# Kernel optimization log

Measured on AMD Instinct MI355X. Metric: run time of the kernel, lower is better.

The kernel has to match this reference:

```python
import jax, jax.numpy as jnp
import numpy as np

D_MODEL = 1024
D_STATE = 16
D_CONV = 4
BATCH = 2
SEQ = 2048


def setup_inputs() -> dict:
    key = jax.random.key(0)
    ks = jax.random.split(key, 10)
    s = lambda fan_in: 1.0 / np.sqrt(fan_in)
    x = jax.random.normal(ks[0], (BATCH, SEQ, D_MODEL), dtype=jnp.float32)
    W_in = jax.random.normal(ks[1], (D_MODEL, 2 * D_MODEL), dtype=jnp.float32) * s(D_MODEL)
    conv_w = jax.random.normal(ks[2], (D_MODEL, D_CONV), dtype=jnp.float32) * s(D_CONV)
    conv_b = jax.random.normal(ks[3], (D_MODEL,), dtype=jnp.float32) * 0.01
    W_x = jax.random.normal(ks[4], (D_MODEL, 2 * D_STATE), dtype=jnp.float32) * s(D_MODEL)
    W_dt = jax.random.normal(ks[5], (D_MODEL, D_MODEL), dtype=jnp.float32) * s(D_MODEL)
    b_dt = jax.random.normal(ks[6], (D_MODEL,), dtype=jnp.float32) * 0.01
    A_log = jax.random.normal(ks[7], (D_MODEL,), dtype=jnp.float32) * 0.1
    D_param = jnp.ones((D_MODEL,), dtype=jnp.float32)
    W_out = jax.random.normal(ks[8], (D_MODEL, D_MODEL), dtype=jnp.float32) * s(D_MODEL)
    return {"x": x, "W_in": W_in, "conv_w": conv_w, "conv_b": conv_b,
            "W_x": W_x, "W_dt": W_dt, "b_dt": b_dt, "A_log": A_log,
            "D_param": D_param, "W_out": W_out}


def _selective_scan(x, A, dt, B, C):
    # x, dt: [b, l, d]; A: [d]; B, C: [b, l, n]
    b, l, d = x.shape
    n = B.shape[-1]
    h0 = jnp.zeros((b, d, n), dtype=x.dtype)

    def step(h, inp):
        x_t, dt_t, B_t, C_t = inp  # [b,d], [b,d], [b,n], [b,n]
        dA = jnp.exp(dt_t * A)[..., None]            # [b, d, 1]
        h = h * dA + x_t[..., None] * B_t[:, None, :]  # [b, d, n]
        y_t = jnp.einsum('bdn,bn->bd', h, C_t)
        return h, y_t

    xs = (jnp.swapaxes(x, 0, 1), jnp.swapaxes(dt, 0, 1),
          jnp.swapaxes(B, 0, 1), jnp.swapaxes(C, 0, 1))
    _, ys = jax.lax.scan(step, h0, xs)               # ys: [l, b, d]
    return jnp.swapaxes(ys, 0, 1)


def _forward(x, W_in, conv_w, conv_b, W_x, W_dt, b_dt, A_log, D_param, W_out):
    seq_len = x.shape[1]
    xz = x @ W_in                                     # [b, l, 2d]
    x_ssm, z = jnp.split(xz, 2, axis=-1)
    # causal depthwise conv (torch pads both sides then slices -> left pad only)
    xc = jnp.swapaxes(x_ssm, 1, 2)                    # [b, d, l]
    kernel = conv_w[:, None, :]                       # [d, 1, k]
    xc = jax.lax.conv_general_dilated(
        xc, kernel, window_strides=(1,), padding=[(D_CONV - 1, 0)],
        dimension_numbers=('NCH', 'OIH', 'NCH'), feature_group_count=D_MODEL)
    xc = xc + conv_b[None, :, None]
    x_ssm = jnp.swapaxes(xc, 1, 2)[:, :seq_len]       # [b, l, d]
    x_ssm = jax.nn.silu(x_ssm)
    A = -jnp.exp(A_log)
    dt = jax.nn.softplus(x_ssm @ W_dt + b_dt)
    BC = x_ssm @ W_x
    B, C = jnp.split(BC, 2, axis=-1)
    y = _selective_scan(x_ssm, A, dt, B, C)
    y = y + x_ssm * D_param
    y = y * jax.nn.silu(z)
    return y @ W_out


def reference(x, W_in, conv_w, conv_b, W_x, W_dt, b_dt, A_log, D_param, W_out):
    return _forward(x, W_in, conv_w, conv_b, W_x, W_dt, b_dt, A_log, D_param, W_out)
```

## Files before the change

### kernel.cpp

```cpp
#include <hip/hip_runtime.h>
#include <hip/hip_bf16.h>
#include <math.h>

#define D_MODEL 1024
#define D_STATE 16
#define D_CONV  4
#define BATCH   2
#define SEQ     2048
#define MROWS   (BATCH * SEQ)
#define CHUNK   32
#define NCHUNK  (SEQ / CHUNK)

typedef __attribute__((ext_vector_type(8))) short bf16x8;
typedef __attribute__((ext_vector_type(4))) float f32x4;

__device__ __forceinline__ unsigned short f2bf(float f) {
    unsigned int u = __builtin_bit_cast(unsigned int, f);
    u = (u + 0x7fffu + ((u >> 16) & 1u)) >> 16;
    return (unsigned short)u;
}
__device__ __forceinline__ float bf2f(unsigned short u) {
    return __builtin_bit_cast(float, (unsigned int)u << 16);
}
__device__ __forceinline__ float softplus_f(float v) {
    return (v > 20.f) ? v : log1pf(expf(v));
}

__device__ __forceinline__ void gl2lds16(const unsigned short* g, unsigned short* l) {
    __builtin_amdgcn_global_load_lds(
        (__attribute__((address_space(1))) void*)(void*)g,
        (__attribute__((address_space(3))) void*)(void*)l, 16, 0, 0);
}

__global__ __launch_bounds__(256) void cvt_bf16(const float* __restrict__ src,
                                                unsigned short* __restrict__ dst) {
    const size_t i = ((size_t)blockIdx.x * 256 + threadIdx.x) * 8;
    const float4 v0 = *(const float4*)(src + i);
    const float4 v1 = *(const float4*)(src + i + 4);
    bf16x8 o;
    o[0] = (short)f2bf(v0.x); o[1] = (short)f2bf(v0.y);
    o[2] = (short)f2bf(v0.z); o[3] = (short)f2bf(v0.w);
    o[4] = (short)f2bf(v1.x); o[5] = (short)f2bf(v1.y);
    o[6] = (short)f2bf(v1.z); o[7] = (short)f2bf(v1.w);
    *(bf16x8*)(dst + i) = o;
}

__global__ __launch_bounds__(256) void wtrans(const float* __restrict__ W,
                                              unsigned short* __restrict__ Wt,
                                              int K, int N) {
    __shared__ float tile[32][33];
    const int n0 = blockIdx.x * 32, k0 = blockIdx.y * 32;
    const int tx = threadIdx.x & 31, ty = threadIdx.x >> 5;
#pragma unroll
    for (int r = 0; r < 4; ++r)
        tile[ty + r * 8][tx] = W[(size_t)(k0 + ty + r * 8) * N + n0 + tx];
    __syncthreads();
#pragma unroll
    for (int r = 0; r < 4; ++r)
        Wt[(size_t)(n0 + ty + r * 8) * K + k0 + tx] = f2bf(tile[tx][ty + r * 8]);
}

__global__ __launch_bounds__(256) void wx_stage(const float* __restrict__ Wx,
                                                unsigned short* __restrict__ Wt_cat) {
    const int idx = blockIdx.x * 256 + threadIdx.x;
    const int k = idx & 1023;
    const int n = idx >> 10;
    unsigned short v = 0;
    if (n < 32) v = f2bf(Wx[(size_t)k * 32 + n]);
    Wt_cat[(size_t)(1024 + n) * 1024 + k] = v;
}

template <int EPI>
__global__ __launch_bounds__(256) void gemm64(
        const unsigned short* __restrict__ A, const unsigned short* __restrict__ Bt,
        void* __restrict__ Cout, int N, int K,
        const float* __restrict__ bias, const float* __restrict__ alog,
        float* __restrict__ bc) {
    __shared__ unsigned short As[2][64 * 32];
    __shared__ unsigned short Bs[2][128 * 32];

    const int tid  = threadIdx.x;
    const int wave = tid >> 6, lane = tid & 63;
    const int q = lane >> 4, mr = lane & 15;
    const int m0 = blockIdx.y * 64, n0 = blockIdx.x * 128;

    f32x4 acc[4][2];
#pragma unroll
    for (int mi = 0; mi < 4; ++mi)
#pragma unroll
        for (int ni = 0; ni < 2; ++ni) acc[mi][ni] = {0.f, 0.f, 0.f, 0.f};

    const int kb = (tid & 3) * 8;
    const unsigned short* Ag  = A + (size_t)(m0 + (tid >> 2)) * K + kb;
    const unsigned short* Bg0 = Bt + (size_t)(n0 + (tid >> 2)) * K + kb;
    const unsigned short* Bg1 = Bt + (size_t)(n0 + ((tid + 256) >> 2)) * K + kb;
    const int sA = tid * 8, sB0 = tid * 8, sB1 = (tid + 256) * 8;

    const int NK = K >> 5;
    gl2lds16(Ag, As[0] + sA);
    gl2lds16(Bg0, Bs[0] + sB0);
    gl2lds16(Bg1, Bs[0] + sB1);

    for (int i = 0; i < NK; ++i) {
        __syncthreads();
        const int cur = i & 1, nxt = cur ^ 1;
        if (i + 1 < NK) {
            const int ko = (i + 1) * 32;
            gl2lds16(Ag + ko, As[nxt] + sA);
            gl2lds16(Bg0 + ko, Bs[nxt] + sB0);
            gl2lds16(Bg1 + ko, Bs[nxt] + sB1);
        }
        bf16x8 af[4], bfr[2];
#pragma unroll
        for (int mi = 0; mi < 4; ++mi)
            af[mi] = *(const bf16x8*)(As[cur] + (mi * 16 + mr) * 32 + q * 8);
#pragma unroll
        for (int ni = 0; ni < 2; ++ni)
            bfr[ni] = *(const bf16x8*)(Bs[cur] + (wave * 32 + ni * 16 + mr) * 32 + q * 8);
#pragma unroll
        for (int mi = 0; mi < 4; ++mi)
#pragma unroll
            for (int ni = 0; ni < 2; ++ni)
                acc[mi][ni] = __builtin_amdgcn_mfma_f32_16x16x32_bf16(
                    af[mi], bfr[ni], acc[mi][ni], 0, 0, 0);
    }

#pragma unroll
    for (int ni = 0; ni < 2; ++ni) {
        const int col = n0 + wave * 32 + ni * 16 + mr;
        float be = 0.f, al = 0.f;
        if (EPI == 3 && col < 1024) { be = bias[col]; al = alog[col]; }
#pragma unroll
        for (int mi = 0; mi < 4; ++mi) {
            const int row0 = m0 + mi * 16 + q * 4;
#pragma unroll
            for (int r = 0; r < 4; ++r) {
                float v = acc[mi][ni][r];
                const int row = row0 + r;
                if (EPI == 0) {
                    ((float*)Cout)[(size_t)row * N + col] = v;
                } else if (EPI == 2) {
                    ((unsigned short*)Cout)[(size_t)row * N + col] = f2bf(v);
                } else {
                    if (col < 1024) {
                        float dt = softplus_f(v + be);
                        ((float*)Cout)[(size_t)row * 1024 + col] = expf(dt * (-expf(al)));
                    } else if (col < 1056) {
                        bc[(size_t)row * 32 + (col - 1024)] = v;
                    }
                }
            }
        }
    }
}

__global__ __launch_bounds__(256) void conv_silu_kernel(
        const unsigned short* __restrict__ xz, const float* __restrict__ conv_w,
        const float* __restrict__ conv_b, unsigned short* __restrict__ xssm) {
    int idx = blockIdx.x * 256 + threadIdx.x;
    int d4 = idx & 255;
    int bt = idx >> 8;
    int t  = bt & (SEQ - 1);
    int d  = d4 * 4;

    float acc[4];
#pragma unroll
    for (int i = 0; i < 4; ++i) acc[i] = conv_b[d + i];

#pragma unroll
    for (int j = 0; j < D_CONV; ++j) {
        int tt = t - (D_CONV - 1) + j;
        if (tt < 0) continue;
        const ushort4 xv = *(const ushort4*)(&xz[((size_t)(bt - t + tt)) * 2048 + d]);
        acc[0] += bf2f(xv.x) * conv_w[(d + 0) * 4 + j];
        acc[1] += bf2f(xv.y) * conv_w[(d + 1) * 4 + j];
        acc[2] += bf2f(xv.z) * conv_w[(d + 2) * 4 + j];
        acc[3] += bf2f(xv.w) * conv_w[(d + 3) * 4 + j];
    }
    ushort4 o;
    o.x = f2bf(acc[0] / (1.f + expf(-acc[0])));
    o.y = f2bf(acc[1] / (1.f + expf(-acc[1])));
    o.z = f2bf(acc[2] / (1.f + expf(-acc[2])));
    o.w = f2bf(acc[3] / (1.f + expf(-acc[3])));
    *(ushort4*)(&xssm[(size_t)bt * D_MODEL + d]) = o;
}

__global__ __launch_bounds__(256) void scan_pass1(
        const unsigned short* __restrict__ xssm, const float* __restrict__ dAb,
        const float* __restrict__ BCb,
        float* __restrict__ Sbuf, float* __restrict__ Pbuf) {
    const int ch = blockIdx.x, dg = blockIdx.y, b = blockIdx.z;
    const int tid = threadIdx.x;
    const int dd  = dg * 256 + tid;
    const int t0  = ch * CHUNK;

    __shared__ float Bs[CHUNK][16];
    if (tid < CHUNK * 4) {
        const int t = tid >> 2, j = (tid & 3) * 4;
        *(float4*)&Bs[t][j] = *(const float4*)&BCb[((size_t)b * SEQ + t0 + t) * 32 + j];
    }
    __syncthreads();

    const size_t base = ((size_t)b * SEQ + t0) * D_MODEL + dd;
    float h[16];
#pragma unroll
    for (int n = 0; n < 16; ++n) h[n] = 0.f;
    float P = 1.f;

#pragma unroll 2
    for (int t = 0; t < CHUNK; ++t) {
        const float dA = dAb[base + (size_t)t * D_MODEL];
        const float x  = bf2f(xssm[base + (size_t)t * D_MODEL]);
        P *= dA;
        const float4 B0 = *(const float4*)&Bs[t][0];
        const float4 B1 = *(const float4*)&Bs[t][4];
        const float4 B2 = *(const float4*)&Bs[t][8];
        const float4 B3 = *(const float4*)&Bs[t][12];
        h[0]  = h[0]  * dA + x * B0.x;  h[1]  = h[1]  * dA + x * B0.y;
        h[2]  = h[2]  * dA + x * B0.z;  h[3]  = h[3]  * dA + x * B0.w;
        h[4]  = h[4]  * dA + x * B1.x;  h[5]  = h[5]  * dA + x * B1.y;
        h[6]  = h[6]  * dA + x * B1.z;  h[7]  = h[7]  * dA + x * B1.w;
        h[8]  = h[8]  * dA + x * B2.x;  h[9]  = h[9]  * dA + x * B2.y;
        h[10] = h[10] * dA + x * B2.z;  h[11] = h[11] * dA + x * B2.w;
        h[12] = h[12] * dA + x * B3.x;  h[13] = h[13] * dA + x * B3.y;
        h[14] = h[14] * dA + x * B3.z;  h[15] = h[15] * dA + x * B3.w;
    }

    const size_t so = ((size_t)(b * D_MODEL + dd) * NCHUNK + ch) * 16;
#pragma unroll
    for (int n = 0; n < 16; n += 4)
        *(float4*)&Sbuf[so + n] = make_float4(h[n], h[n + 1], h[n + 2], h[n + 3]);
    Pbuf[(size_t)(b * D_MODEL + dd) * NCHUNK + ch] = P;
}

__global__ __launch_bounds__(128) void scan_mid(
        const float* __restrict__ Sbuf, const float* __restrict__ Pbuf,
        float* __restrict__ Hin) {
    const int idx = blockIdx.x * 128 + threadIdx.x;
    const int n   = idx & 15;
    const int dn  = idx >> 4;

    float h = 0.f;
    for (int ch = 0; ch < NCHUNK; ++ch) {
        const size_t s = ((size_t)dn * NCHUNK + ch) * 16 + n;
        Hin[s] = h;
        h = Pbuf[(size_t)dn * NCHUNK + ch] * h + Sbuf[s];
    }
}

__global__ __launch_bounds__(256) void scan_pass2(
        const unsigned short* __restrict__ xssm, const float* __restrict__ dAb,
        const float* __restrict__ BCb, const unsigned short* __restrict__ xz,
        const float* __restrict__ Dp, const float* __restrict__ Hin,
        unsigned short* __restrict__ ybuf) {
    const int ch = blockIdx.x, dg = blockIdx.y, b = blockIdx.z;
    const int tid = threadIdx.x;
    const int dd  = dg * 256 + tid;
    const int t0  = ch * CHUNK;

    __shared__ float BCs[CHUNK][32];
    {
        const int t = tid >> 3, j = (tid & 7) * 4;
        *(float4*)&BCs[t][j] = *(const float4*)&BCb[((size_t)b * SEQ + t0 + t) * 32 + j];
    }
    __syncthreads();

    const float Dpv = Dp[dd];
    const size_t base  = ((size_t)b * SEQ + t0) * D_MODEL + dd;
    const size_t baseZ = ((size_t)b * SEQ + t0) * 2048 + D_MODEL + dd;

    float h[16];
    const size_t ho = ((size_t)(b * D_MODEL + dd) * NCHUNK + ch) * 16;
#pragma unroll
    for (int n = 0; n < 16; n += 4) {
        const float4 hv = *(const float4*)&Hin[ho + n];
        h[n] = hv.x; h[n + 1] = hv.y; h[n + 2] = hv.z; h[n + 3] = hv.w;
    }

#pragma unroll 2
    for (int t = 0; t < CHUNK; ++t) {
        const float dA = dAb[base + (size_t)t * D_MODEL];
        const float x  = bf2f(xssm[base + (size_t)t * D_MODEL]);
        const float4 B0 = *(const float4*)&BCs[t][0];
        const float4 B1 = *(const float4*)&BCs[t][4];
        const float4 B2 = *(const float4*)&BCs[t][8];
        const float4 B3 = *(const float4*)&BCs[t][12];
        const float4 C0 = *(const float4*)&BCs[t][16];
        const float4 C1 = *(const float4*)&BCs[t][20];
        const float4 C2 = *(const float4*)&BCs[t][24];
        const float4 C3 = *(const float4*)&BCs[t][28];
        float y = 0.f;
        h[0]  = h[0]  * dA + x * B0.x;  y += h[0]  * C0.x;
        h[1]  = h[1]  * dA + x * B0.y;  y += h[1]  * C0.y;
        h[2]  = h[2]  * dA + x * B0.z;  y += h[2]  * C0.z;
        h[3]  = h[3]  * dA + x * B0.w;  y += h[3]  * C0.w;
        h[4]  = h[4]  * dA + x * B1.x;  y += h[4]  * C1.x;
        h[5]  = h[5]  * dA + x * B1.y;  y += h[5]  * C1.y;
        h[6]  = h[6]  * dA + x * B1.z;  y += h[6]  * C1.z;
        h[7]  = h[7]  * dA + x * B1.w;  y += h[7]  * C1.w;
        h[8]  = h[8]  * dA + x * B2.x;  y += h[8]  * C2.x;
        h[9]  = h[9]  * dA + x * B2.y;  y += h[9]  * C2.y;
        h[10] = h[10] * dA + x * B2.z;  y += h[10] * C2.z;
        h[11] = h[11] * dA + x * B2.w;  y += h[11] * C2.w;
        h[12] = h[12] * dA + x * B3.x;  y += h[12] * C3.x;
        h[13] = h[13] * dA + x * B3.y;  y += h[13] * C3.y;
        h[14] = h[14] * dA + x * B3.z;  y += h[14] * C3.z;
        h[15] = h[15] * dA + x * B3.w;  y += h[15] * C3.w;

        const float zv = bf2f(xz[baseZ + (size_t)t * 2048]);
        const float sz = zv / (1.f + expf(-zv));
        ybuf[base + (size_t)t * D_MODEL] = f2bf((y + x * Dpv) * sz);
    }
}

extern "C" void kernel_launch(void* const* d_in, const int* in_sizes, int n_in,
                              void* d_out, int out_size, void* d_ws, size_t ws_size,
                              hipStream_t stream) {
    const float* x       = (const float*)d_in[0];
    const float* W_in    = (const float*)d_in[1];
    const float* conv_w  = (const float*)d_in[2];
    const float* conv_b  = (const float*)d_in[3];
    const float* W_x     = (const float*)d_in[4];
    const float* W_dt    = (const float*)d_in[5];
    const float* b_dt    = (const float*)d_in[6];
    const float* A_log   = (const float*)d_in[7];
    const float* D_param = (const float*)d_in[8];
    const float* W_out   = (const float*)d_in[9];
    float* out = (float*)d_out;
    char* ws   = (char*)d_ws;

    unsigned short* xz_bf   = (unsigned short*)(ws + 0);
    unsigned short* xssm_bf = (unsigned short*)(ws + 16777216);
    float*          dAb     = (float*)(ws + 25165824);
    float*          BCb     = (float*)(ws + 41943040);
    unsigned short* ybuf_bf = (unsigned short*)(ws + 42467328);
    unsigned short* xb      = (unsigned short*)(ws + 50855936);
    unsigned short* Wt_in   = (unsigned short*)(ws + 59244544);
    unsigned short* Wt_cat  = (unsigned short*)(ws + 63438848);
    unsigned short* Wt_out  = (unsigned short*)(ws + 65798144);
    float*          Sbuf    = (float*)(ws + 67895296);
    float*          Pbuf    = (float*)(ws + 76283904);
    float*          Hin     = (float*)(ws + 76808192);

    cvt_bf16<<<MROWS * D_MODEL / (256 * 8), 256, 0, stream>>>(x, xb);
    wtrans<<<dim3(2048 / 32, 1024 / 32), 256, 0, stream>>>(W_in, Wt_in, 1024, 2048);
    wtrans<<<dim3(1024 / 32, 1024 / 32), 256, 0, stream>>>(W_dt, Wt_cat, 1024, 1024);
    wx_stage<<<(128 * 1024) / 256, 256, 0, stream>>>(W_x, Wt_cat);
    wtrans<<<dim3(1024 / 32, 1024 / 32), 256, 0, stream>>>(W_out, Wt_out, 1024, 1024);

    gemm64<2><<<dim3(2048 / 128, MROWS / 64), 256, 0, stream>>>(
        xb, Wt_in, xz_bf, 2048, D_MODEL, nullptr, nullptr, nullptr);
    conv_silu_kernel<<<(MROWS * 256) / 256, 256, 0, stream>>>(xz_bf, conv_w, conv_b, xssm_bf);
    gemm64<3><<<dim3(1152 / 128, MROWS / 64), 256, 0, stream>>>(
        xssm_bf, Wt_cat, dAb, 1152, D_MODEL, b_dt, A_log, BCb);
    scan_pass1<<<dim3(NCHUNK, D_MODEL / 256, BATCH), 256, 0, stream>>>(
        xssm_bf, dAb, BCb, Sbuf, Pbuf);
    scan_mid<<<(BATCH * D_MODEL * 16) / 128, 128, 0, stream>>>(Sbuf, Pbuf, Hin);
    scan_pass2<<<dim3(NCHUNK, D_MODEL / 256, BATCH), 256, 0, stream>>>(
        xssm_bf, dAb, BCb, xz_bf, D_param, Hin, ybuf_bf);
    gemm64<0><<<dim3(1024 / 128, MROWS / 64), 256, 0, stream>>>(
        ybuf_bf, Wt_out, out, D_MODEL, D_MODEL, nullptr, nullptr, nullptr);
}
```

Baseline: 276.1 us.

## Store decay factors in bf16, batch scan loads, transpose chunk-state layout, widen conv

The dt-projection epilogue now writes exp(dt*A) as bf16 instead of fp32, halving the traffic of the largest intermediate, which both scan passes read. The scan loops now issue eight timesteps of loads before computing, which raises memory-level parallelism. The chunk-state buffers move to a chunk-major layout so scan_mid's per-chunk accesses are coalesced across threads. The conv kernel handles eight channels per thread with vector loads. The cost is reduced precision in the decay factor, whose error compounds over long scans.

After: 253.9 us. 8.0% less time.

```diff
diff --git a/kernel.cpp b/kernel.cpp
--- a/kernel.cpp
+++ b/kernel.cpp
@@ -10,6 +10,7 @@
 #define MROWS   (BATCH * SEQ)
 #define CHUNK   32
 #define NCHUNK  (SEQ / CHUNK)
+#define BD      (BATCH * D_MODEL)
 
 typedef __attribute__((ext_vector_type(8))) short bf16x8;
 typedef __attribute__((ext_vector_type(4))) float f32x4;
@@ -144,7 +145,8 @@
                 } else {
                     if (col < 1024) {
                         float dt = softplus_f(v + be);
-                        ((float*)Cout)[(size_t)row * 1024 + col] = expf(dt * (-expf(al)));
+                        ((unsigned short*)Cout)[(size_t)row * 1024 + col] =
+                            f2bf(expf(dt * (-expf(al))));
                     } else if (col < 1056) {
                         bc[(size_t)row * 32 + (col - 1024)] = v;
                     }
@@ -157,36 +159,52 @@
 __global__ __launch_bounds__(256) void conv_silu_kernel(
         const unsigned short* __restrict__ xz, const float* __restrict__ conv_w,
         const float* __restrict__ conv_b, unsigned short* __restrict__ xssm) {
-    int idx = blockIdx.x * 256 + threadIdx.x;
-    int d4 = idx & 255;
-    int bt = idx >> 8;
-    int t  = bt & (SEQ - 1);
-    int d  = d4 * 4;
-
-    float acc[4];
-#pragma unroll
-    for (int i = 0; i < 4; ++i) acc[i] = conv_b[d + i];
+    const int idx = blockIdx.x * 256 + threadIdx.x;
+    const int d8 = idx & 127;
+    const int bt = idx >> 7;
+    const int t  = bt & (SEQ - 1);
+    const int d  = d8 * 8;
+
+    float4 w[8];
+#pragma unroll
+    for (int i = 0; i < 8; ++i) w[i] = *(const float4*)&conv_w[(d + i) * 4];
+
+    float acc[8];
+    {
+        const float4 b0 = *(const float4*)&conv_b[d];
+        const float4 b1 = *(const float4*)&conv_b[d + 4];
+        acc[0] = b0.x; acc[1] = b0.y; acc[2] = b0.z; acc[3] = b0.w;
+        acc[4] = b1.x; acc[5] = b1.y; acc[6] = b1.z; acc[7] = b1.w;
+    }
 
 #pragma unroll
     for (int j = 0; j < D_CONV; ++j) {
-        int tt = t - (D_CONV - 1) + j;
+        const int tt = t - (D_CONV - 1) + j;
         if (tt < 0) continue;
-        const ushort4 xv = *(const ushort4*)(&xz[((size_t)(bt - t + tt)) * 2048 + d]);
-        acc[0] += bf2f(xv.x) * conv_w[(d + 0) * 4 + j];
-        acc[1] += bf2f(xv.y) * conv_w[(d + 1) * 4 + j];
-        acc[2] += bf2f(xv.z) * conv_w[(d + 2) * 4 + j];
-        acc[3] += bf2f(xv.w) * conv_w[(d + 3) * 4 + j];
-    }
-    ushort4 o;
-    o.x = f2bf(acc[0] / (1.f + expf(-acc[0])));
-    o.y = f2bf(acc[1] / (1.f + expf(-acc[1])));
-    o.z = f2bf(acc[2] / (1.f + expf(-acc[2])));
-    o.w = f2bf(acc[3] / (1.f + expf(-acc[3])));
-    *(ushort4*)(&xssm[(size_t)bt * D_MODEL + d]) = o;
+        const bf16x8 xv = *(const bf16x8*)(&xz[((size_t)(bt - t + tt)) * 2048 + d]);
+        const float wj[8] = {j == 0 ? w[0].x : j == 1 ? w[0].y : j == 2 ? w[0].z : w[0].w,
+                             j == 0 ? w[1].x : j == 1 ? w[1].y : j == 2 ? w[1].z : w[1].w,
+                             j == 0 ? w[2].x : j == 1 ? w[2].y : j == 2 ? w[2].z : w[2].w,
+                             j == 0 ? w[3].x : j == 1 ? w[3].y : j == 2 ? w[3].z : w[3].w,
+                             j == 0 ? w[4].x : j == 1 ? w[4].y : j == 2 ? w[4].z : w[4].w,
+                             j == 0 ? w[5].x : j == 1 ? w[5].y : j == 2 ? w[5].z : w[5].w,
+                             j == 0 ? w[6].x : j == 1 ? w[6].y : j == 2 ? w[6].z : w[6].w,
+                             j == 0 ? w[7].x : j == 1 ? w[7].y : j == 2 ? w[7].z : w[7].w};
+#pragma unroll
+        for (int i = 0; i < 8; ++i)
+            acc[i] += bf2f((unsigned short)xv[i]) * wj[i];
+    }
+    bf16x8 o;
+#pragma unroll
+    for (int i = 0; i < 8; ++i) {
+        const float s = acc[i] / (1.f + expf(-acc[i]));
+        o[i] = (short)f2bf(s);
+    }
+    *(bf16x8*)(&xssm[(size_t)bt * D_MODEL + d]) = o;
 }
 
 __global__ __launch_bounds__(256) void scan_pass1(
-        const unsigned short* __restrict__ xssm, const float* __restrict__ dAb,
+        const unsigned short* __restrict__ xssm, const unsigned short* __restrict__ dA16,
         const float* __restrict__ BCb,
         float* __restrict__ Sbuf, float* __restrict__ Pbuf) {
     const int ch = blockIdx.x, dg = blockIdx.y, b = blockIdx.z;
@@ -207,30 +225,40 @@
     for (int n = 0; n < 16; ++n) h[n] = 0.f;
     float P = 1.f;
 
-#pragma unroll 2
-    for (int t = 0; t < CHUNK; ++t) {
-        const float dA = dAb[base + (size_t)t * D_MODEL];
-        const float x  = bf2f(xssm[base + (size_t)t * D_MODEL]);
-        P *= dA;
-        const float4 B0 = *(const float4*)&Bs[t][0];
-        const float4 B1 = *(const float4*)&Bs[t][4];
-        const float4 B2 = *(const float4*)&Bs[t][8];
-        const float4 B3 = *(const float4*)&Bs[t][12];
-        h[0]  = h[0]  * dA + x * B0.x;  h[1]  = h[1]  * dA + x * B0.y;
-        h[2]  = h[2]  * dA + x * B0.z;  h[3]  = h[3]  * dA + x * B0.w;
-        h[4]  = h[4]  * dA + x * B1.x;  h[5]  = h[5]  * dA + x * B1.y;
-        h[6]  = h[6]  * dA + x * B1.z;  h[7]  = h[7]  * dA + x * B1.w;
-        h[8]  = h[8]  * dA + x * B2.x;  h[9]  = h[9]  * dA + x * B2.y;
-        h[10] = h[10] * dA + x * B2.z;  h[11] = h[11] * dA + x * B2.w;
-        h[12] = h[12] * dA + x * B3.x;  h[13] = h[13] * dA + x * B3.y;
-        h[14] = h[14] * dA + x * B3.z;  h[15] = h[15] * dA + x * B3.w;
-    }
-
-    const size_t so = ((size_t)(b * D_MODEL + dd) * NCHUNK + ch) * 16;
+    for (int g = 0; g < CHUNK; g += 8) {
+        float dAr[8], xr[8];
+#pragma unroll
+        for (int p = 0; p < 8; ++p) {
+            const size_t o = base + (size_t)(g + p) * D_MODEL;
+            dAr[p] = bf2f(dA16[o]);
+            xr[p]  = bf2f(xssm[o]);
+        }
+#pragma unroll
+        for (int p = 0; p < 8; ++p) {
+            const int t = g + p;
+            const float dA = dAr[p], x = xr[p];
+            P *= dA;
+            const float4 B0 = *(const float4*)&Bs[t][0];
+            const float4 B1 = *(const float4*)&Bs[t][4];
+            const float4 B2 = *(const float4*)&Bs[t][8];
+            const float4 B3 = *(const float4*)&Bs[t][12];
+            h[0]  = h[0]  * dA + x * B0.x;  h[1]  = h[1]  * dA + x * B0.y;
+            h[2]  = h[2]  * dA + x * B0.z;  h[3]  = h[3]  * dA + x * B0.w;
+            h[4]  = h[4]  * dA + x * B1.x;  h[5]  = h[5]  * dA + x * B1.y;
+            h[6]  = h[6]  * dA + x * B1.z;  h[7]  = h[7]  * dA + x * B1.w;
+            h[8]  = h[8]  * dA + x * B2.x;  h[9]  = h[9]  * dA + x * B2.y;
+            h[10] = h[10] * dA + x * B2.z;  h[11] = h[11] * dA + x * B2.w;
+            h[12] = h[12] * dA + x * B3.x;  h[13] = h[13] * dA + x * B3.y;
+            h[14] = h[14] * dA + x * B3.z;  h[15] = h[15] * dA + x * B3.w;
+        }
+    }
+
+    const int dn = b * D_MODEL + dd;
+    const size_t so = ((size_t)ch * BD + dn) * 16;
 #pragma unroll
     for (int n = 0; n < 16; n += 4)
         *(float4*)&Sbuf[so + n] = make_float4(h[n], h[n + 1], h[n + 2], h[n + 3]);
-    Pbuf[(size_t)(b * D_MODEL + dd) * NCHUNK + ch] = P;
+    Pbuf[(size_t)ch * BD + dn] = P;
 }
 
 __global__ __launch_bounds__(128) void scan_mid(
@@ -242,14 +270,14 @@
 
     float h = 0.f;
     for (int ch = 0; ch < NCHUNK; ++ch) {
-        const size_t s = ((size_t)dn * NCHUNK + ch) * 16 + n;
+        const size_t s = ((size_t)ch * BD + dn) * 16 + n;
         Hin[s] = h;
-        h = Pbuf[(size_t)dn * NCHUNK + ch] * h + Sbuf[s];
+        h = Pbuf[(size_t)ch * BD + dn] * h + Sbuf[s];
     }
 }
 
 __global__ __launch_bounds__(256) void scan_pass2(
-        const unsigned short* __restrict__ xssm, const float* __restrict__ dAb,
+        const unsigned short* __restrict__ xssm, const unsigned short* __restrict__ dA16,
         const float* __restrict__ BCb, const unsigned short* __restrict__ xz,
         const float* __restrict__ Dp, const float* __restrict__ Hin,
         unsigned short* __restrict__ ybuf) {
@@ -270,46 +298,57 @@
     const size_t baseZ = ((size_t)b * SEQ + t0) * 2048 + D_MODEL + dd;
 
     float h[16];
-    const size_t ho = ((size_t)(b * D_MODEL + dd) * NCHUNK + ch) * 16;
+    const int dn = b * D_MODEL + dd;
+    const size_t ho = ((size_t)ch * BD + dn) * 16;
 #pragma unroll
     for (int n = 0; n < 16; n += 4) {
         const float4 hv = *(const float4*)&Hin[ho + n];
         h[n] = hv.x; h[n + 1] = hv.y; h[n + 2] = hv.z; h[n + 3] = hv.w;
     }
 
-#pragma unroll 2
-    for (int t = 0; t < CHUNK; ++t) {
-        const float dA = dAb[base + (size_t)t * D_MODEL];
-        const float x  = bf2f(xssm[base + (size_t)t * D_MODEL]);
-        const float4 B0 = *(const float4*)&BCs[t][0];
-        const float4 B1 = *(const float4*)&BCs[t][4];
-        const float4 B2 = *(const float4*)&BCs[t][8];
-        const float4 B3 = *(const float4*)&BCs[t][12];
-        const float4 C0 = *(const float4*)&BCs[t][16];
-        const float4 C1 = *(const float4*)&BCs[t][20];
-        const float4 C2 = *(const float4*)&BCs[t][24];
-        const float4 C3 = *(const float4*)&BCs[t][28];
-        float y = 0.f;
-        h[0]  = h[0]  * dA + x * B0.x;  y += h[0]  * C0.x;
-        h[1]  = h[1]  * dA + x * B0.y;  y += h[1]  * C0.y;
-        h[2]  = h[2]  * dA + x * B0.z;  y += h[2]  * C0.z;
-        h[3]  = h[3]  * dA + x * B0.w;  y += h[3]  * C0.w;
-        h[4]  = h[4]  * dA + x * B1.x;  y += h[4]  * C1.x;
-        h[5]  = h[5]  * dA + x * B1.y;  y += h[5]  * C1.y;
-        h[6]  = h[6]  * dA + x * B1.z;  y += h[6]  * C1.z;
-        h[7]  = h[7]  * dA + x * B1.w;  y += h[7]  * C1.w;
-        h[8]  = h[8]  * dA + x * B2.x;  y += h[8]  * C2.x;
-        h[9]  = h[9]  * dA + x * B2.y;  y += h[9]  * C2.y;
-        h[10] = h[10] * dA + x * B2.z;  y += h[10] * C2.z;
-        h[11] = h[11] * dA + x * B2.w;  y += h[11] * C2.w;
-        h[12] = h[12] * dA + x * B3.x;  y += h[12] * C3.x;
-        h[13] = h[13] * dA + x * B3.y;  y += h[13] * C3.y;
-        h[14] = h[14] * dA + x * B3.z;  y += h[14] * C3.z;
-        h[15] = h[15] * dA + x * B3.w;  y += h[15] * C3.w;
-
-        const float zv = bf2f(xz[baseZ + (size_t)t * 2048]);
-        const float sz = zv / (1.f + expf(-zv));
-        ybuf[base + (size_t)t * D_MODEL] = f2bf((y + x * Dpv) * sz);
+    for (int g = 0; g < CHUNK; g += 8) {
+        float dAr[8], xr[8], zr[8];
+#pragma unroll
+        for (int p = 0; p < 8; ++p) {
+            const size_t o = base + (size_t)(g + p) * D_MODEL;
+            dAr[p] = bf2f(dA16[o]);
+            xr[p]  = bf2f(xssm[o]);
+            zr[p]  = bf2f(xz[baseZ + (size_t)(g + p) * 2048]);
+        }
+#pragma unroll
+        for (int p = 0; p < 8; ++p) {
+            const int t = g + p;
+            const float dA = dAr[p], x = xr[p];
+            const float4 B0 = *(const float4*)&BCs[t][0];
+            const float4 B1 = *(const float4*)&BCs[t][4];
+            const float4 B2 = *(const float4*)&BCs[t][8];
+            const float4 B3 = *(const float4*)&BCs[t][12];
+            const float4 C0 = *(const float4*)&BCs[t][16];
+            const float4 C1 = *(const float4*)&BCs[t][20];
+            const float4 C2 = *(const float4*)&BCs[t][24];
+            const float4 C3 = *(const float4*)&BCs[t][28];
+            float y = 0.f;
+            h[0]  = h[0]  * dA + x * B0.x;  y += h[0]  * C0.x;
+            h[1]  = h[1]  * dA + x * B0.y;  y += h[1]  * C0.y;
+            h[2]  = h[2]  * dA + x * B0.z;  y += h[2]  * C0.z;
+            h[3]  = h[3]  * dA + x * B0.w;  y += h[3]  * C0.w;
+            h[4]  = h[4]  * dA + x * B1.x;  y += h[4]  * C1.x;
+            h[5]  = h[5]  * dA + x * B1.y;  y += h[5]  * C1.y;
+            h[6]  = h[6]  * dA + x * B1.z;  y += h[6]  * C1.z;
+            h[7]  = h[7]  * dA + x * B1.w;  y += h[7]  * C1.w;
+            h[8]  = h[8]  * dA + x * B2.x;  y += h[8]  * C2.x;
+            h[9]  = h[9]  * dA + x * B2.y;  y += h[9]  * C2.y;
+            h[10] = h[10] * dA + x * B2.z;  y += h[10] * C2.z;
+            h[11] = h[11] * dA + x * B2.w;  y += h[11] * C2.w;
+            h[12] = h[12] * dA + x * B3.x;  y += h[12] * C3.x;
+            h[13] = h[13] * dA + x * B3.y;  y += h[13] * C3.y;
+            h[14] = h[14] * dA + x * B3.z;  y += h[14] * C3.z;
+            h[15] = h[15] * dA + x * B3.w;  y += h[15] * C3.w;
+
+            const float zv = zr[p];
+            const float sz = zv / (1.f + expf(-zv));
+            ybuf[base + (size_t)t * D_MODEL] = f2bf((y + x * Dpv) * sz);
+        }
     }
 }
 
@@ -331,7 +370,7 @@
 
     unsigned short* xz_bf   = (unsigned short*)(ws + 0);
     unsigned short* xssm_bf = (unsigned short*)(ws + 16777216);
-    float*          dAb     = (float*)(ws + 25165824);
+    unsigned short* dAb16   = (unsigned short*)(ws + 25165824);
     float*          BCb     = (float*)(ws + 41943040);
     unsigned short* ybuf_bf = (unsigned short*)(ws + 42467328);
     unsigned short* xb      = (unsigned short*)(ws + 50855936);
@@ -350,14 +389,14 @@
 
     gemm64<2><<<dim3(2048 / 128, MROWS / 64), 256, 0, stream>>>(
         xb, Wt_in, xz_bf, 2048, D_MODEL, nullptr, nullptr, nullptr);
-    conv_silu_kernel<<<(MROWS * 256) / 256, 256, 0, stream>>>(xz_bf, conv_w, conv_b, xssm_bf);
+    conv_silu_kernel<<<(MROWS * 128) / 256, 256, 0, stream>>>(xz_bf, conv_w, conv_b, xssm_bf);
     gemm64<3><<<dim3(1152 / 128, MROWS / 64), 256, 0, stream>>>(
-        xssm_bf, Wt_cat, dAb, 1152, D_MODEL, b_dt, A_log, BCb);
+        xssm_bf, Wt_cat, dAb16, 1152, D_MODEL, b_dt, A_log, BCb);
     scan_pass1<<<dim3(NCHUNK, D_MODEL / 256, BATCH), 256, 0, stream>>>(
-        xssm_bf, dAb, BCb, Sbuf, Pbuf);
-    scan_mid<<<(BATCH * D_MODEL * 16) / 128, 128, 0, stream>>>(Sbuf, Pbuf, Hin);
+        xssm_bf, dAb16, BCb, Sbuf, Pbuf);
+    scan_mid<<<(BD * 16) / 128, 128, 0, stream>>>(Sbuf, Pbuf, Hin);
     scan_pass2<<<dim3(NCHUNK, D_MODEL / 256, BATCH), 256, 0, stream>>>(
-        xssm_bf, dAb, BCb, xz_bf, D_param, Hin, ybuf_bf);
+        xssm_bf, dAb16, BCb, xz_bf, D_param, Hin, ybuf_bf);
     gemm64<0><<<dim3(1024 / 128, MROWS / 64), 256, 0, stream>>>(
         ybuf_bf, Wt_out, out, D_MODEL, D_MODEL, nullptr, nullptr, nullptr);
 }
```
